# Kernel tuning notes

Hardware: AMD Instinct MI355X
Metric: run time of the kernel (lower is better)

Reference implementation:

```python
import jax, jax.numpy as jnp
import numpy as np

B, N, VF, EF, DV, DE, LN = 64, 64, 32, 16, 128, 128, 4
EPS_INNER = 128.0  # BatchNorm1d(MAX_N, internal_d_vert): 2nd positional arg is eps (faithful to source bug)
EPS_BN = 1e-5


def gev_layer(v_in, e_in, evW, evb, eW, eb, vW, vb, relu=True):
    act = jax.nn.relu if relu else (lambda x: x)
    ev = v_in @ evW + evb                                   # [B,N,De]
    # outer_v_sum: ev.unsqueeze(1) + ev.unsqueeze(2) -> [B,N,N,De]
    e_out = act(e_in @ eW + eb + ev[:, None, :, :] + ev[:, :, None, :])
    per_v_e = e_out.sum(axis=1)                             # sum-aggregate over dim 1
    v_out = act(jnp.concatenate([per_v_e, v_in], axis=-1) @ vW + vb)
    return v_out, e_out


def bn_flat(v, g, b):
    # BatchNorm1d(N*VF) on [B, N*VF] in training mode (biased var)
    x = v.reshape(-1, N * VF)
    mu = x.mean(axis=0)
    var = x.var(axis=0)
    x = (x - mu) * jax.lax.rsqrt(var + EPS_BN) * g + b
    return x.reshape(-1, N, VF)


def bn_inner(v, g, b):
    # BatchNorm1d(MAX_N, eps=128) on [B, N, D]: channels are the N axis, stats over (B, D)
    mu = v.mean(axis=(0, 2), keepdims=True)
    var = v.var(axis=(0, 2), keepdims=True)
    return (v - mu) * jax.lax.rsqrt(var + EPS_INNER) * g[None, :, None] + b[None, :, None]


def setup_inputs() -> dict:
    key = jax.random.key(0)
    ks = jax.random.split(key, 24)
    s = 0.01  # force_lin_init with init_noise=0.01, biases zero
    nrm = lambda k, shp: jax.random.normal(k, shp, dtype=jnp.float32) * s
    inp = {
        "v": jax.random.normal(ks[0], (B, N, VF), dtype=jnp.float32),
        "e": jax.random.normal(ks[1], (B, N, N, EF), dtype=jnp.float32),
        "bn_in_g": jnp.ones((N * VF,), jnp.float32),
        "bn_in_b": jnp.zeros((N * VF,), jnp.float32),
        "g1_evW": nrm(ks[2], (VF, DE)), "g1_evb": jnp.zeros((DE,), jnp.float32),
        "g1_eW": nrm(ks[3], (EF, DE)), "g1_eb": jnp.zeros((DE,), jnp.float32),
        "g1_vW": nrm(ks[4], (VF + DE, DV)), "g1_vb": jnp.zeros((DV,), jnp.float32),
        "inn_evW": nrm(ks[5], (LN, DV, DE)), "inn_evb": jnp.zeros((LN, DE), jnp.float32),
        "inn_eW": nrm(ks[6], (LN, DE, DE)), "inn_eb": jnp.zeros((LN, DE), jnp.float32),
        "inn_vW": nrm(ks[7], (LN, DV + DE, DV)), "inn_vb": jnp.zeros((LN, DV), jnp.float32),
        "bn_g": jnp.ones((LN, N), jnp.float32),
        "bn_b": jnp.zeros((LN, N), jnp.float32),
        "g3_evW": nrm(ks[8], (DV, 1)), "g3_evb": jnp.zeros((1,), jnp.float32),
        "g3_eW": nrm(ks[9], (DE, 1)), "g3_eb": jnp.zeros((1,), jnp.float32),
        "g3_vW": nrm(ks[10], (DV + 1, 1)), "g3_vb": jnp.zeros((1,), jnp.float32),
    }
    return inp


def reference(v, e, bn_in_g, bn_in_b, g1_evW, g1_evb, g1_eW, g1_eb, g1_vW, g1_vb,
              inn_evW, inn_evb, inn_eW, inn_eb, inn_vW, inn_vb, bn_g, bn_b,
              g3_evW, g3_evb, g3_eW, g3_eb, g3_vW, g3_vb):
    v = bn_flat(v, bn_in_g, bn_in_b)
    v, e = gev_layer(v, e, g1_evW, g1_evb, g1_eW, g1_eb, g1_vW, g1_vb)
    for i in range(LN):
        v_next, e_next = gev_layer(v, e, inn_evW[i], inn_evb[i], inn_eW[i], inn_eb[i], inn_vW[i], inn_vb[i])
        v = v_next + v  # resnet
        e = e_next + e
        v = bn_inner(v, bn_g[i], bn_b[i])
    v, e = gev_layer(v, e, g3_evW, g3_evb, g3_eW, g3_eb, g3_vW, g3_vb, relu=False)
    return v, e
```

## Files before the change

kernel.cpp:

```cpp
#include <hip/hip_runtime.h>
#include <hip/hip_bf16.h>


typedef __bf16 bf16_t;
typedef __bf16 bf16x8 __attribute__((ext_vector_type(8)));
typedef float f32x4 __attribute__((ext_vector_type(4)));

__global__ __launch_bounds__(256) void k_bn_in(const float* __restrict__ vin,
    const float* __restrict__ g, const float* __restrict__ bt,
    float* __restrict__ v0) {
  int ch = blockIdx.x * 256 + threadIdx.x;
  float s = 0.f, s2 = 0.f;
  for (int b = 0; b < 64; ++b) { float x = vin[b * 2048 + ch]; s += x; s2 += x * x; }
  float mu = s * (1.f / 64.f);
  float var = s2 * (1.f / 64.f) - mu * mu;
  float sc = rsqrtf(var + 1e-5f) * g[ch];
  float bb = bt[ch];
  for (int b = 0; b < 64; ++b) {
    float x = vin[b * 2048 + ch];
    v0[b * 2048 + ch] = (x - mu) * sc + bb;
  }
}

__global__ __launch_bounds__(256) void k_prep_wt(const float* __restrict__ eW,
    bf16_t* __restrict__ Wt) {
  int idx = blockIdx.x * 256 + threadIdx.x;
  int l = idx >> 14, r = idx & 16383, n = r >> 7, k = r & 127;
  Wt[idx] = (bf16_t)eW[(l << 14) + (k << 7) + n];
}

template <int K>
__global__ __launch_bounds__(128) void k_ev(const float* __restrict__ v_in,
    const float* __restrict__ W, const float* __restrict__ bias,
    float* __restrict__ out) {
  __shared__ float rows[8][K];
  const int r0 = blockIdx.x * 8;
  const int c = threadIdx.x;
  for (int idx = c; idx < 8 * K; idx += 128) {
    int rr = idx / K, kk = idx % K;
    rows[rr][kk] = v_in[(r0 + rr) * K + kk];
  }
  __syncthreads();
  float acc[8];
  const float bv = bias[c];
#pragma unroll
  for (int r = 0; r < 8; ++r) acc[r] = bv;
  for (int k4 = 0; k4 < K; k4 += 4) {
    float w0 = W[(k4 + 0) * 128 + c], w1 = W[(k4 + 1) * 128 + c];
    float w2 = W[(k4 + 2) * 128 + c], w3 = W[(k4 + 3) * 128 + c];
#pragma unroll
    for (int r = 0; r < 8; ++r) {
      float4 x = *(const float4*)&rows[r][k4];
      acc[r] += x.x * w0 + x.y * w1 + x.z * w2 + x.w * w3;
    }
  }
#pragma unroll
  for (int r = 0; r < 8; ++r) out[(r0 + r) * 128 + c] = acc[r];
}

__global__ __launch_bounds__(256) void k_edge_g1(const float* __restrict__ e0,
    const float* __restrict__ eW, const float* __restrict__ eb,
    const float* __restrict__ ev, bf16_t* __restrict__ e_ws,
    float* __restrict__ pve) {
  __shared__ float A0[64][16];
  __shared__ float Wg[16][128];
  __shared__ float evj[128];
  __shared__ float psum[2][128];
  const int b = blockIdx.x >> 6, j = blockIdx.x & 63;
  const int tid = threadIdx.x;
  {
    int rr = tid >> 2, seg = tid & 3;
    int gi = ((b * 64 + rr) * 64 + j) * 16 + seg * 4;
    *(float4*)&A0[rr][seg * 4] = *(const float4*)&e0[gi];
  }
  for (int idx = tid; idx < 512; idx += 256) {
    int k = idx >> 5, cs = (idx & 31) * 4;
    *(float4*)&Wg[k][cs] = *(const float4*)&eW[k * 128 + cs];
  }
  if (tid < 128) evj[tid] = eb[tid] + ev[(b * 64 + j) * 128 + tid];
  __syncthreads();
  const int c = tid & 127, half = tid >> 7;
  float ps = 0.f;
  for (int ii = 0; ii < 32; ++ii) {
    int i = half * 32 + ii;
    float acc = evj[c] + ev[(b * 64 + i) * 128 + c];
#pragma unroll
    for (int k = 0; k < 16; ++k) acc += A0[i][k] * Wg[k][c];
    acc = fmaxf(acc, 0.f);
    ps += acc;
    e_ws[((b * 64 + i) * 64 + j) * 128 + c] = (bf16_t)acc;
  }
  psum[half][c] = ps;
  __syncthreads();
  if (tid < 128) pve[(b * 64 + j) * 128 + tid] = psum[0][tid] + psum[1][tid];
}

__global__ __launch_bounds__(128) void k_v_g1(const float* __restrict__ pve,
    const float* __restrict__ v0, const float* __restrict__ vW,
    const float* __restrict__ vb, float* __restrict__ v) {
  __shared__ float in[8][160];
  const int r0 = blockIdx.x * 8;
  const int c = threadIdx.x;
#pragma unroll
  for (int t = 0; t < 8; ++t) {
    int idx = c + t * 128;
    int rr = idx >> 7, k = idx & 127;
    in[rr][k] = pve[(r0 + rr) * 128 + k];
  }
#pragma unroll
  for (int t = 0; t < 2; ++t) {
    int idx = c + t * 128;
    int rr = idx >> 5, k = idx & 31;
    in[rr][128 + k] = v0[(r0 + rr) * 32 + k];
  }
  __syncthreads();
  float acc[8];
  const float bv = vb[c];
#pragma unroll
  for (int r = 0; r < 8; ++r) acc[r] = bv;
  for (int k4 = 0; k4 < 160; k4 += 4) {
    float w0 = vW[(k4 + 0) * 128 + c], w1 = vW[(k4 + 1) * 128 + c];
    float w2 = vW[(k4 + 2) * 128 + c], w3 = vW[(k4 + 3) * 128 + c];
#pragma unroll
    for (int r = 0; r < 8; ++r) {
      float4 x = *(const float4*)&in[r][k4];
      acc[r] += x.x * w0 + x.y * w1 + x.z * w2 + x.w * w3;
    }
  }
#pragma unroll
  for (int r = 0; r < 8; ++r) v[(r0 + r) * 128 + c] = fmaxf(acc[r], 0.f);
}

__global__ __launch_bounds__(256) void k_edge_inner(bf16_t* __restrict__ e_ws,
    const bf16_t* __restrict__ Wt, const float* __restrict__ eb,
    const float* __restrict__ ev, float* __restrict__ pve) {
  __shared__ bf16_t As[64][136];
  __shared__ bf16_t Ws[128][136];
  __shared__ float evj[128];
  const int b = blockIdx.x >> 6, j = blockIdx.x & 63;
  const int tid = threadIdx.x;
#pragma unroll
  for (int t = 0; t < 4; ++t) {
    int idx = tid + t * 256;
    int row = idx >> 4, seg = (idx & 15) * 8;
    int gi = ((b * 64 + row) * 64 + j) * 128 + seg;
    *(int4*)&As[row][seg] = *(const int4*)&e_ws[gi];
  }
#pragma unroll
  for (int t = 0; t < 8; ++t) {
    int idx = tid + t * 256;
    int row = idx >> 4, seg = (idx & 15) * 8;
    *(int4*)&Ws[row][seg] = *(const int4*)&Wt[row * 128 + seg];
  }
  if (tid < 128) evj[tid] = eb[tid] + ev[(b * 64 + j) * 128 + tid];
  __syncthreads();
  const int lane = tid & 63, wave = tid >> 6;
  const int quad = lane >> 4, l16 = lane & 15;
  const int nbase = wave * 32;
  f32x4 acc[4][2];
#pragma unroll
  for (int mt = 0; mt < 4; ++mt)
#pragma unroll
    for (int nt = 0; nt < 2; ++nt) acc[mt][nt] = (f32x4){0.f, 0.f, 0.f, 0.f};
#pragma unroll
  for (int ks = 0; ks < 4; ++ks) {
    const int k0 = ks * 32 + quad * 8;
    bf16x8 av[4], bv[2];
#pragma unroll
    for (int mt = 0; mt < 4; ++mt) av[mt] = *(const bf16x8*)&As[mt * 16 + l16][k0];
#pragma unroll
    for (int nt = 0; nt < 2; ++nt) bv[nt] = *(const bf16x8*)&Ws[nbase + nt * 16 + l16][k0];
#pragma unroll
    for (int mt = 0; mt < 4; ++mt)
#pragma unroll
      for (int nt = 0; nt < 2; ++nt)
        acc[mt][nt] = __builtin_amdgcn_mfma_f32_16x16x32_bf16(av[mt], bv[nt], acc[mt][nt], 0, 0, 0);
  }
  __syncthreads();
  float ps[2] = {0.f, 0.f};
#pragma unroll
  for (int nt = 0; nt < 2; ++nt) {
    const int c = nbase + nt * 16 + l16;
    const float ej = evj[c];
#pragma unroll
    for (int mt = 0; mt < 4; ++mt) {
#pragma unroll
      for (int reg = 0; reg < 4; ++reg) {
        const int i = mt * 16 + quad * 4 + reg;
        float val = acc[mt][nt][reg] + ej + ev[(b * 64 + i) * 128 + c];
        val = fmaxf(val, 0.f);
        ps[nt] += val;
        float eo = (float)As[i][c];
        As[i][c] = (bf16_t)(val + eo);
      }
    }
  }
#pragma unroll
  for (int nt = 0; nt < 2; ++nt) {
    float p = ps[nt];
    p += __shfl_xor(p, 16);
    p += __shfl_xor(p, 32);
    if (quad == 0) pve[(b * 64 + j) * 128 + nbase + nt * 16 + l16] = p;
  }
  __syncthreads();
#pragma unroll
  for (int t = 0; t < 4; ++t) {
    int idx = tid + t * 256;
    int row = idx >> 4, seg = (idx & 15) * 8;
    int gi = ((b * 64 + row) * 64 + j) * 128 + seg;
    *(int4*)&e_ws[gi] = *(const int4*)&As[row][seg];
  }
}

__global__ __launch_bounds__(128) void k_v_inner(const float* __restrict__ pve,
    float* __restrict__ v, const float* __restrict__ vW,
    const float* __restrict__ vb, float* __restrict__ stats) {
  __shared__ float in[8][256];
  __shared__ float outs[8][132];
  const int r0 = blockIdx.x * 8;
  const int c = threadIdx.x;
#pragma unroll
  for (int t = 0; t < 8; ++t) {
    int idx = c + t * 128;
    int rr = idx >> 7, k = idx & 127;
    in[rr][k] = pve[(r0 + rr) * 128 + k];
    in[rr][128 + k] = v[(r0 + rr) * 128 + k];
  }
  __syncthreads();
  float acc[8];
  const float bv = vb[c];
#pragma unroll
  for (int r = 0; r < 8; ++r) acc[r] = bv;
  for (int k4 = 0; k4 < 256; k4 += 4) {
    float w0 = vW[(k4 + 0) * 128 + c], w1 = vW[(k4 + 1) * 128 + c];
    float w2 = vW[(k4 + 2) * 128 + c], w3 = vW[(k4 + 3) * 128 + c];
#pragma unroll
    for (int r = 0; r < 8; ++r) {
      float4 x = *(const float4*)&in[r][k4];
      acc[r] += x.x * w0 + x.y * w1 + x.z * w2 + x.w * w3;
    }
  }
#pragma unroll
  for (int r = 0; r < 8; ++r) {
    float val = fmaxf(acc[r], 0.f) + in[r][128 + c];
    outs[r][c] = val;
    v[(r0 + r) * 128 + c] = val;
  }
  __syncthreads();
  if (c < 8) {
    float s = 0.f, s2 = 0.f;
    for (int k = 0; k < 128; ++k) { float x = outs[c][k]; s += x; s2 += x * x; }
    int n = (r0 + c) & 63;
    atomicAdd(&stats[n], s);
    atomicAdd(&stats[64 + n], s2);
  }
}

__global__ __launch_bounds__(256) void k_bn_apply(float* __restrict__ v,
    const float* __restrict__ stats, const float* __restrict__ g,
    const float* __restrict__ bt) {
  int idx = blockIdx.x * 256 + threadIdx.x;
  int n = (idx >> 7) & 63;
  float mu = stats[n] * (1.f / 8192.f);
  float var = stats[64 + n] * (1.f / 8192.f) - mu * mu;
  float sc = rsqrtf(var + 128.f) * g[n];
  v[idx] = (v[idx] - mu) * sc + bt[n];
}

__global__ __launch_bounds__(256) void k_ev3(const float* __restrict__ v,
    const float* __restrict__ W, const float* __restrict__ bias,
    float* __restrict__ ev3) {
  int r = blockIdx.x * 4 + (threadIdx.x >> 6);
  int lane = threadIdx.x & 63;
  float acc = v[r * 128 + lane] * W[lane] + v[r * 128 + 64 + lane] * W[64 + lane];
#pragma unroll
  for (int m = 1; m < 64; m <<= 1) acc += __shfl_xor(acc, m);
  if (lane == 0) ev3[r] = acc + bias[0];
}

__global__ __launch_bounds__(256) void k_edge_g3(const bf16_t* __restrict__ e_ws,
    const float* __restrict__ eW3, const float* __restrict__ eb3,
    const float* __restrict__ ev3, float* __restrict__ out_e,
    float* __restrict__ pve3) {
  __shared__ float W3[128];
  const int b = blockIdx.x >> 6, i = blockIdx.x & 63;
  const int tid = threadIdx.x;
  if (tid < 128) W3[tid] = eW3[tid];
  __syncthreads();
  const int j = tid >> 2, cs = (tid & 3) * 32;
  const bf16_t* ep = &e_ws[(size_t)((b * 64 + i) * 64 + j) * 128 + cs];
  float acc = 0.f;
#pragma unroll
  for (int t = 0; t < 4; ++t) {
    bf16x8 x = *(const bf16x8*)&ep[t * 8];
#pragma unroll
    for (int u = 0; u < 8; ++u) acc += (float)x[u] * W3[cs + t * 8 + u];
  }
  acc += __shfl_xor(acc, 1);
  acc += __shfl_xor(acc, 2);
  if ((tid & 3) == 0) {
    float s = acc + eb3[0] + ev3[b * 64 + i] + ev3[b * 64 + j];
    out_e[(b * 64 + i) * 64 + j] = s;
    atomicAdd(&pve3[b * 64 + j], s);
  }
}

__global__ __launch_bounds__(256) void k_v_g3(const float* __restrict__ v,
    const float* __restrict__ pve3, const float* __restrict__ vW,
    const float* __restrict__ vb, float* __restrict__ out_v) {
  int r = blockIdx.x * 4 + (threadIdx.x >> 6);
  int lane = threadIdx.x & 63;
  float acc = v[r * 128 + lane] * vW[1 + lane] + v[r * 128 + 64 + lane] * vW[65 + lane];
#pragma unroll
  for (int m = 1; m < 64; m <<= 1) acc += __shfl_xor(acc, m);
  if (lane == 0) out_v[r] = acc + pve3[r] * vW[0] + vb[0];
}

extern "C" void kernel_launch(void* const* d_in, const int* in_sizes, int n_in,
                              void* d_out, int out_size, void* d_ws, size_t ws_size,
                              hipStream_t stream) {
  const float* in_v    = (const float*)d_in[0];
  const float* in_e    = (const float*)d_in[1];
  const float* bn_in_g = (const float*)d_in[2];
  const float* bn_in_b = (const float*)d_in[3];
  const float* g1_evW  = (const float*)d_in[4];
  const float* g1_evb  = (const float*)d_in[5];
  const float* g1_eW   = (const float*)d_in[6];
  const float* g1_eb   = (const float*)d_in[7];
  const float* g1_vW   = (const float*)d_in[8];
  const float* g1_vb   = (const float*)d_in[9];
  const float* inn_evW = (const float*)d_in[10];
  const float* inn_evb = (const float*)d_in[11];
  const float* inn_eW  = (const float*)d_in[12];
  const float* inn_eb  = (const float*)d_in[13];
  const float* inn_vW  = (const float*)d_in[14];
  const float* inn_vb  = (const float*)d_in[15];
  const float* bn_g    = (const float*)d_in[16];
  const float* bn_b    = (const float*)d_in[17];
  const float* g3_evW  = (const float*)d_in[18];
  const float* g3_evb  = (const float*)d_in[19];
  const float* g3_eW   = (const float*)d_in[20];
  const float* g3_eb   = (const float*)d_in[21];
  const float* g3_vW   = (const float*)d_in[22];
  const float* g3_vb   = (const float*)d_in[23];

  char* ws = (char*)d_ws;
  bf16_t* e_ws = (bf16_t*)(ws);
  float* v     = (float*)(ws + 67108864);
  float* ev    = (float*)(ws + 69206016);
  float* pve   = (float*)(ws + 71303168);
  float* v0    = (float*)(ws + 73400320);
  bf16_t* Wt   = (bf16_t*)(ws + 73924608);
  float* ev3   = (float*)(ws + 74055680);
  float* pve3  = (float*)(ws + 74072064);
  float* stats = (float*)(ws + 74088448);

  float* out_v = (float*)d_out;
  float* out_e = (float*)d_out + 4096;

  k_bn_in<<<8, 256, 0, stream>>>(in_v, bn_in_g, bn_in_b, v0);
  k_prep_wt<<<256, 256, 0, stream>>>(inn_eW, Wt);

  k_ev<32><<<512, 128, 0, stream>>>(v0, g1_evW, g1_evb, ev);
  k_edge_g1<<<4096, 256, 0, stream>>>(in_e, g1_eW, g1_eb, ev, e_ws, pve);
  k_v_g1<<<512, 128, 0, stream>>>(pve, v0, g1_vW, g1_vb, v);

  for (int l = 0; l < 4; ++l) {
    k_ev<128><<<512, 128, 0, stream>>>(v, inn_evW + l * 16384, inn_evb + l * 128, ev);
    k_edge_inner<<<4096, 256, 0, stream>>>(e_ws, Wt + l * 16384, inn_eb + l * 128, ev, pve);
    hipMemsetAsync(stats, 0, 512, stream);
    k_v_inner<<<512, 128, 0, stream>>>(pve, v, inn_vW + l * 32768, inn_vb + l * 128, stats);
    k_bn_apply<<<2048, 256, 0, stream>>>(v, stats, bn_g + l * 64, bn_b + l * 64);
  }

  k_ev3<<<1024, 256, 0, stream>>>(v, g3_evW, g3_evb, ev3);
  hipMemsetAsync(pve3, 0, 16384, stream);
  k_edge_g3<<<4096, 256, 0, stream>>>(e_ws, g3_eW, g3_eb, ev3, out_e, pve3);
  k_v_g3<<<1024, 256, 0, stream>>>(v, pve3, g3_vW, g3_vb, out_v);
}
```

Baseline: 449.5 us.

## Use MFMA in first edge layer and keep edge weights in registers

The first edge layer's scalar 16-wide FP32 dot product becomes a bf16 MFMA with K zero-padded to 32, and its output is staged through LDS for coalesced stores. Both edge kernels swap MFMA operands so the accumulator holds four consecutive channels per lane, which allows vectorised ev, eb and pve accesses. Edge weights are loaded straight from global memory into registers instead of a 128x136 LDS tile, reducing LDS use per block. The inner kernel also prefetches the residual edge values into registers and issues the tile loads before the barrier to overlap memory latency. The cost is more register pressure, and the first layer now rounds its input and weights to bf16.

```diff
diff --git a/kernel.cpp b/kernel.cpp
--- a/kernel.cpp
+++ b/kernel.cpp
@@ -4,6 +4,7 @@
 
 typedef __bf16 bf16_t;
 typedef __bf16 bf16x8 __attribute__((ext_vector_type(8)));
+typedef __bf16 bf16x4 __attribute__((ext_vector_type(4)));
 typedef float f32x4 __attribute__((ext_vector_type(4)));
 
 __global__ __launch_bounds__(256) void k_bn_in(const float* __restrict__ vin,
@@ -62,37 +63,79 @@
     const float* __restrict__ eW, const float* __restrict__ eb,
     const float* __restrict__ ev, bf16_t* __restrict__ e_ws,
     float* __restrict__ pve) {
-  __shared__ float A0[64][16];
-  __shared__ float Wg[16][128];
-  __shared__ float evj[128];
-  __shared__ float psum[2][128];
+  __shared__ bf16_t A0s[64][40];
+  __shared__ bf16_t Os[64][136];
   const int b = blockIdx.x >> 6, j = blockIdx.x & 63;
   const int tid = threadIdx.x;
+  const int lane = tid & 63, w = tid >> 6;
+  const int quad = lane >> 4, l16 = lane & 15;
   {
-    int rr = tid >> 2, seg = tid & 3;
-    int gi = ((b * 64 + rr) * 64 + j) * 16 + seg * 4;
-    *(float4*)&A0[rr][seg * 4] = *(const float4*)&e0[gi];
-  }
-  for (int idx = tid; idx < 512; idx += 256) {
-    int k = idx >> 5, cs = (idx & 31) * 4;
-    *(float4*)&Wg[k][cs] = *(const float4*)&eW[k * 128 + cs];
-  }
-  if (tid < 128) evj[tid] = eb[tid] + ev[(b * 64 + j) * 128 + tid];
-  __syncthreads();
-  const int c = tid & 127, half = tid >> 7;
-  float ps = 0.f;
-  for (int ii = 0; ii < 32; ++ii) {
-    int i = half * 32 + ii;
-    float acc = evj[c] + ev[(b * 64 + i) * 128 + c];
-#pragma unroll
-    for (int k = 0; k < 16; ++k) acc += A0[i][k] * Wg[k][c];
-    acc = fmaxf(acc, 0.f);
-    ps += acc;
-    e_ws[((b * 64 + i) * 64 + j) * 128 + c] = (bf16_t)acc;
-  }
-  psum[half][c] = ps;
-  __syncthreads();
-  if (tid < 128) pve[(b * 64 + j) * 128 + tid] = psum[0][tid] + psum[1][tid];
+    int row = tid >> 2, s = (tid & 3) * 4;
+    f32x4 x = *(const f32x4*)&e0[((b * 64 + row) * 64 + j) * 16 + s];
+    bf16x4 y;
+#pragma unroll
+    for (int r = 0; r < 4; ++r) y[r] = (bf16_t)x[r];
+    *(bf16x4*)&A0s[row][s] = y;
+    bf16x4 z = {(bf16_t)0.f, (bf16_t)0.f, (bf16_t)0.f, (bf16_t)0.f};
+    *(bf16x4*)&A0s[row][16 + s] = z;
+  }
+  const int c0[2] = {w * 32 + quad * 4, w * 32 + 16 + quad * 4};
+  bf16x8 wf[2];
+#pragma unroll
+  for (int nt = 0; nt < 2; ++nt) {
+    const int c = w * 32 + nt * 16 + l16;
+#pragma unroll
+    for (int jj = 0; jj < 8; ++jj)
+      wf[nt][jj] = (quad < 2) ? (bf16_t)eW[(quad * 8 + jj) * 128 + c] : (bf16_t)0.f;
+  }
+  f32x4 acc[4][2];
+#pragma unroll
+  for (int nt = 0; nt < 2; ++nt) {
+    f32x4 e1 = *(const f32x4*)&eb[c0[nt]];
+    f32x4 e2 = *(const f32x4*)&ev[(b * 64 + j) * 128 + c0[nt]];
+    f32x4 ej = e1 + e2;
+#pragma unroll
+    for (int mt = 0; mt < 4; ++mt) acc[mt][nt] = ej;
+  }
+  __syncthreads();
+#pragma unroll
+  for (int mt = 0; mt < 4; ++mt) {
+    bf16x8 ef = *(const bf16x8*)&A0s[mt * 16 + l16][quad * 8];
+#pragma unroll
+    for (int nt = 0; nt < 2; ++nt)
+      acc[mt][nt] = __builtin_amdgcn_mfma_f32_16x16x32_bf16(wf[nt], ef, acc[mt][nt], 0, 0, 0);
+  }
+#pragma unroll
+  for (int nt = 0; nt < 2; ++nt) {
+    f32x4 ps = {0.f, 0.f, 0.f, 0.f};
+#pragma unroll
+    for (int mt = 0; mt < 4; ++mt) {
+      const int i = mt * 16 + l16;
+      f32x4 evi = *(const f32x4*)&ev[(b * 64 + i) * 128 + c0[nt]];
+      f32x4 val = acc[mt][nt] + evi;
+      bf16x4 outv;
+#pragma unroll
+      for (int r = 0; r < 4; ++r) {
+        float vv = fmaxf(val[r], 0.f);
+        ps[r] += vv;
+        outv[r] = (bf16_t)vv;
+      }
+      *(bf16x4*)&Os[i][c0[nt]] = outv;
+    }
+#pragma unroll
+    for (int m = 1; m <= 8; m <<= 1) {
+#pragma unroll
+      for (int r = 0; r < 4; ++r) ps[r] += __shfl_xor(ps[r], m);
+    }
+    if (l16 == 0) *(f32x4*)&pve[(b * 64 + j) * 128 + c0[nt]] = ps;
+  }
+  __syncthreads();
+#pragma unroll
+  for (int t = 0; t < 4; ++t) {
+    int idx = tid + t * 256;
+    int row = idx >> 4, seg = (idx & 15) * 8;
+    *(int4*)&e_ws[((b * 64 + row) * 64 + j) * 128 + seg] = *(const int4*)&Os[row][seg];
+  }
 }
 
 __global__ __launch_bounds__(128) void k_v_g1(const float* __restrict__ pve,
@@ -135,80 +178,89 @@
     const bf16_t* __restrict__ Wt, const float* __restrict__ eb,
     const float* __restrict__ ev, float* __restrict__ pve) {
   __shared__ bf16_t As[64][136];
-  __shared__ bf16_t Ws[128][136];
-  __shared__ float evj[128];
   const int b = blockIdx.x >> 6, j = blockIdx.x & 63;
   const int tid = threadIdx.x;
+  const int lane = tid & 63, w = tid >> 6;
+  const int quad = lane >> 4, l16 = lane & 15;
+  int4 stg[4];
 #pragma unroll
   for (int t = 0; t < 4; ++t) {
     int idx = tid + t * 256;
     int row = idx >> 4, seg = (idx & 15) * 8;
-    int gi = ((b * 64 + row) * 64 + j) * 128 + seg;
-    *(int4*)&As[row][seg] = *(const int4*)&e_ws[gi];
-  }
-#pragma unroll
-  for (int t = 0; t < 8; ++t) {
-    int idx = tid + t * 256;
-    int row = idx >> 4, seg = (idx & 15) * 8;
-    *(int4*)&Ws[row][seg] = *(const int4*)&Wt[row * 128 + seg];
-  }
-  if (tid < 128) evj[tid] = eb[tid] + ev[(b * 64 + j) * 128 + tid];
-  __syncthreads();
-  const int lane = tid & 63, wave = tid >> 6;
-  const int quad = lane >> 4, l16 = lane & 15;
-  const int nbase = wave * 32;
+    stg[t] = *(const int4*)&e_ws[((b * 64 + row) * 64 + j) * 128 + seg];
+  }
+  bf16x8 wf[2][4];
+#pragma unroll
+  for (int nt = 0; nt < 2; ++nt)
+#pragma unroll
+    for (int ks = 0; ks < 4; ++ks)
+      wf[nt][ks] = *(const bf16x8*)&Wt[(w * 32 + nt * 16 + l16) * 128 + ks * 32 + quad * 8];
+  const int c0[2] = {w * 32 + quad * 4, w * 32 + 16 + quad * 4};
+  bf16x4 eo[4][2];
+#pragma unroll
+  for (int mt = 0; mt < 4; ++mt)
+#pragma unroll
+    for (int nt = 0; nt < 2; ++nt)
+      eo[mt][nt] = *(const bf16x4*)&e_ws[((b * 64 + mt * 16 + l16) * 64 + j) * 128 + c0[nt]];
   f32x4 acc[4][2];
 #pragma unroll
-  for (int mt = 0; mt < 4; ++mt)
-#pragma unroll
-    for (int nt = 0; nt < 2; ++nt) acc[mt][nt] = (f32x4){0.f, 0.f, 0.f, 0.f};
-#pragma unroll
-  for (int ks = 0; ks < 4; ++ks) {
-    const int k0 = ks * 32 + quad * 8;
-    bf16x8 av[4], bv[2];
-#pragma unroll
-    for (int mt = 0; mt < 4; ++mt) av[mt] = *(const bf16x8*)&As[mt * 16 + l16][k0];
-#pragma unroll
-    for (int nt = 0; nt < 2; ++nt) bv[nt] = *(const bf16x8*)&Ws[nbase + nt * 16 + l16][k0];
-#pragma unroll
-    for (int mt = 0; mt < 4; ++mt)
-#pragma unroll
-      for (int nt = 0; nt < 2; ++nt)
-        acc[mt][nt] = __builtin_amdgcn_mfma_f32_16x16x32_bf16(av[mt], bv[nt], acc[mt][nt], 0, 0, 0);
-  }
-  __syncthreads();
-  float ps[2] = {0.f, 0.f};
-#pragma unroll
   for (int nt = 0; nt < 2; ++nt) {
-    const int c = nbase + nt * 16 + l16;
-    const float ej = evj[c];
-#pragma unroll
-    for (int mt = 0; mt < 4; ++mt) {
-#pragma unroll
-      for (int reg = 0; reg < 4; ++reg) {
-        const int i = mt * 16 + quad * 4 + reg;
-        float val = acc[mt][nt][reg] + ej + ev[(b * 64 + i) * 128 + c];
-        val = fmaxf(val, 0.f);
-        ps[nt] += val;
-        float eo = (float)As[i][c];
-        As[i][c] = (bf16_t)(val + eo);
-      }
-    }
-  }
-#pragma unroll
-  for (int nt = 0; nt < 2; ++nt) {
-    float p = ps[nt];
-    p += __shfl_xor(p, 16);
-    p += __shfl_xor(p, 32);
-    if (quad == 0) pve[(b * 64 + j) * 128 + nbase + nt * 16 + l16] = p;
-  }
-  __syncthreads();
+    f32x4 e1 = *(const f32x4*)&eb[c0[nt]];
+    f32x4 e2 = *(const f32x4*)&ev[(b * 64 + j) * 128 + c0[nt]];
+    f32x4 ej = e1 + e2;
+#pragma unroll
+    for (int mt = 0; mt < 4; ++mt) acc[mt][nt] = ej;
+  }
 #pragma unroll
   for (int t = 0; t < 4; ++t) {
     int idx = tid + t * 256;
     int row = idx >> 4, seg = (idx & 15) * 8;
-    int gi = ((b * 64 + row) * 64 + j) * 128 + seg;
-    *(int4*)&e_ws[gi] = *(const int4*)&As[row][seg];
+    *(int4*)&As[row][seg] = stg[t];
+  }
+  __syncthreads();
+#pragma unroll
+  for (int ks = 0; ks < 4; ++ks) {
+    bf16x8 ef[4];
+#pragma unroll
+    for (int mt = 0; mt < 4; ++mt)
+      ef[mt] = *(const bf16x8*)&As[mt * 16 + l16][ks * 32 + quad * 8];
+#pragma unroll
+    for (int mt = 0; mt < 4; ++mt)
+#pragma unroll
+      for (int nt = 0; nt < 2; ++nt)
+        acc[mt][nt] = __builtin_amdgcn_mfma_f32_16x16x32_bf16(wf[nt][ks], ef[mt], acc[mt][nt], 0, 0, 0);
+  }
+  __syncthreads();
+#pragma unroll
+  for (int nt = 0; nt < 2; ++nt) {
+    f32x4 ps = {0.f, 0.f, 0.f, 0.f};
+#pragma unroll
+    for (int mt = 0; mt < 4; ++mt) {
+      const int i = mt * 16 + l16;
+      f32x4 evi = *(const f32x4*)&ev[(b * 64 + i) * 128 + c0[nt]];
+      f32x4 val = acc[mt][nt] + evi;
+      bf16x4 outv;
+#pragma unroll
+      for (int r = 0; r < 4; ++r) {
+        float vv = fmaxf(val[r], 0.f);
+        ps[r] += vv;
+        outv[r] = (bf16_t)(vv + (float)eo[mt][nt][r]);
+      }
+      *(bf16x4*)&As[i][c0[nt]] = outv;
+    }
+#pragma unroll
+    for (int m = 1; m <= 8; m <<= 1) {
+#pragma unroll
+      for (int r = 0; r < 4; ++r) ps[r] += __shfl_xor(ps[r], m);
+    }
+    if (l16 == 0) *(f32x4*)&pve[(b * 64 + j) * 128 + c0[nt]] = ps;
+  }
+  __syncthreads();
+#pragma unroll
+  for (int t = 0; t < 4; ++t) {
+    int idx = tid + t * 256;
+    int row = idx >> 4, seg = (idx & 15) * 8;
+    *(int4*)&e_ws[((b * 64 + row) * 64 + j) * 128 + seg] = *(const int4*)&As[row][seg];
   }
 }
 
```

New measurement: 535.4 us. +19.1%, slower.
